# Optimization experiments

Hardware: AMD Instinct MI355X
Metric: run time of the kernel (lower is better)

The kernel has to match this reference:

```python
import jax, jax.numpy as jnp
import numpy as np

# Dimensions (match init_kwargs / input_specs)
B, S, F, H = 4, 1024, 1024, 16
D = F // H            # head_dim = 64
MAX_LEN = 1024        # synthesizer random-table length


def setup_inputs() -> dict:
    key = jax.random.key(0)
    ks = jax.random.split(key, 7)
    init = 0.02  # stand-in for lecun-style kernel init scale
    rn = lambda k, shape, sc=init: (jax.random.normal(k, shape, jnp.float32) * sc)
    return {
        "inputs_q": jax.random.normal(ks[0], (B, S, F), jnp.float32),
        "Wq": rn(ks[1], (F, H, D)), "bq": jnp.zeros((H, D), jnp.float32),
        "Wk": rn(ks[2], (F, H, D)), "bk": jnp.zeros((H, D), jnp.float32),
        "Wv": rn(ks[3], (F, H, D)), "bv": jnp.zeros((H, D), jnp.float32),
        "R":  rn(ks[4], (H, MAX_LEN, MAX_LEN)),   # 'random' synthesizer param
        "Wo": rn(ks[5], (H, D, F)), "bo": jnp.zeros((F,), jnp.float32),
    }


def reference(inputs_q, Wq, bq, Wk, bk, Wv, bv, R, Wo, bo):
    # Self-attention: inputs_kv = inputs_q. QKV projections (DenseGeneral axis=-1 -> (H, D)).
    q = jnp.einsum('bqf,fhd->bqhd', inputs_q, Wq) + bq
    k = jnp.einsum('bkf,fhd->bkhd', inputs_q, Wk) + bk
    v = jnp.einsum('bkf,fhd->bkhd', inputs_q, Wv) + bv

    qlen, kvlen = q.shape[1], k.shape[1]
    q = q / jnp.sqrt(jnp.asarray(D, q.dtype))

    # QK^T scores [b, h, q, k] + additive synthetic random weights (broadcast over batch).
    scores = jnp.einsum('bqhd,bkhd->bhqk', q, k) + R[None, :, :qlen, :kvlen]

    # softmax over the attention (kv) axis; deterministic (dropout_rate = 0.0)
    attn = jax.nn.softmax(scores, axis=-1)

    # weighted values, back to [b, q, h, d]
    y = jnp.einsum('bhqk,bkhd->bqhd', attn, v)

    # output DenseGeneral over (heads, head_dim) -> features
    return jnp.einsum('bqhd,hdf->bqf', y, Wo) + bo
```

## Files before the change

kernel.cpp:

```cpp
#include <hip/hip_runtime.h>
#include <hip/hip_bf16.h>

typedef __bf16 bf16;
typedef __bf16 bf16x8 __attribute__((ext_vector_type(8)));
typedef float f32x4 __attribute__((ext_vector_type(4)));

typedef __attribute__((address_space(1))) const void as1_const_void;
typedef __attribute__((address_space(3))) void as3_void;

#define LOG2E 1.44269504088896340736f

__device__ __forceinline__ void gload_lds16(const bf16* g, bf16* l) {
    __builtin_amdgcn_global_load_lds((as1_const_void*)g, (as3_void*)l, 16, 0, 0);
}

__device__ __forceinline__ f32x4 mfma_bf16(bf16x8 a, bf16x8 b, f32x4 c) {
    return __builtin_amdgcn_mfma_f32_16x16x32_bf16(a, b, c, 0, 0, 0);
}

__global__ __launch_bounds__(256) void cvt_f32_bf16(const float* in, bf16* out, int n) {
    int i = (blockIdx.x * 256 + threadIdx.x) * 8;
    if (i >= n) return;
    f32x4 a = *(const f32x4*)(in + i);
    f32x4 b = *(const f32x4*)(in + i + 4);
    bf16x8 o;
#pragma unroll
    for (int j = 0; j < 4; ++j) { o[j] = (bf16)a[j]; o[4 + j] = (bf16)b[j]; }
    *(bf16x8*)(out + i) = o;
}

__global__ __launch_bounds__(256) void transcvt4(const float* i0, const float* i1,
                                                 const float* i2, const float* i3,
                                                 bf16* o0, bf16* o1, bf16* o2, bf16* o3) {
    const float* in;
    bf16* out;
    switch (blockIdx.z) {
        case 0: in = i0; out = o0; break;
        case 1: in = i1; out = o1; break;
        case 2: in = i2; out = o2; break;
        default: in = i3; out = o3; break;
    }
    __shared__ bf16 tile[64][72];
    const int t = threadIdx.x;
    const int r0 = blockIdx.y * 64, c0 = blockIdx.x * 64;
#pragma unroll
    for (int i = 0; i < 4; ++i) {
        int e = t * 4 + i * 1024;
        int r = e >> 6, c = e & 63;
        f32x4 v = *(const f32x4*)(in + (size_t)(r0 + r) * 1024 + c0 + c);
#pragma unroll
        for (int jj = 0; jj < 4; ++jj) tile[c + jj][r] = (bf16)v[jj];
    }
    __syncthreads();
#pragma unroll
    for (int i = 0; i < 2; ++i) {
        int e = t * 8 + i * 2048;
        int r = e >> 6, c = e & 63;
        bf16x8 v;
#pragma unroll
        for (int jj = 0; jj < 8; ++jj) v[jj] = tile[r][c + jj];
        *(bf16x8*)(out + (size_t)(c0 + r) * 1024 + r0 + c) = v;
    }
}

struct GArg { const bf16* BT; const float* bias; void* out; float scale; int mode; };
struct GArgs { GArg g[3]; };

__global__ __launch_bounds__(256) void gemm_bt(const bf16* A, GArgs args, int M, int N, int K) {
    GArg ga = args.g[blockIdx.z];
    __shared__ bf16 As[128 * 32];
    __shared__ bf16 Bs[128 * 32];
    const int t = threadIdx.x;
    const int w = t >> 6, l = t & 63;
    const int fr = l & 15, fq = l >> 4;
    const int brow = blockIdx.y * 128, bcol = blockIdx.x * 128;
    const int wr = w >> 1, wc = w & 1;

    f32x4 acc[4][4] = {};

    const int srow = t >> 2;
    const int scol = (t & 3) * 8;
    const bf16* gA = A + (size_t)(brow + srow) * K + scol;
    const bf16* gB = ga.BT + (size_t)(bcol + srow) * K + scol;

    for (int k0 = 0; k0 < K; k0 += 32) {
        __syncthreads();
        gload_lds16(gA + k0,           As + w * 512);
        gload_lds16(gA + 64 * K + k0,  As + 2048 + w * 512);
        gload_lds16(gB + k0,           Bs + w * 512);
        gload_lds16(gB + 64 * K + k0,  Bs + 2048 + w * 512);
        __syncthreads();

        bf16x8 af[4], bfr[4];
#pragma unroll
        for (int m = 0; m < 4; ++m)
            af[m] = *(const bf16x8*)(As + (wr * 64 + m * 16 + fr) * 32 + fq * 8);
#pragma unroll
        for (int n = 0; n < 4; ++n)
            bfr[n] = *(const bf16x8*)(Bs + (wc * 64 + n * 16 + fr) * 32 + fq * 8);
#pragma unroll
        for (int m = 0; m < 4; ++m)
#pragma unroll
            for (int n = 0; n < 4; ++n)
                acc[m][n] = mfma_bf16(af[m], bfr[n], acc[m][n]);
    }

    float biasv[4];
#pragma unroll
    for (int n = 0; n < 4; ++n)
        biasv[n] = ga.bias[bcol + wc * 64 + n * 16 + fr];

#pragma unroll
    for (int m = 0; m < 4; ++m) {
#pragma unroll
        for (int n = 0; n < 4; ++n) {
            int gcol = bcol + wc * 64 + n * 16 + fr;
#pragma unroll
            for (int j = 0; j < 4; ++j) {
                int grow = brow + wr * 64 + m * 16 + fq * 4 + j;
                float v = (acc[m][n][j] + biasv[n]) * ga.scale;
                if (ga.mode == 0) {
                    ((bf16*)ga.out)[(size_t)grow * N + gcol] = (bf16)v;
                } else if (ga.mode == 1) {
                    int b = grow >> 10, s = grow & 1023;
                    int h = gcol >> 6, d = gcol & 63;
                    ((bf16*)ga.out)[(((size_t)(b * 16 + h)) * 64 + d) * 1024 + s] = (bf16)v;
                } else {
                    ((float*)ga.out)[(size_t)grow * N + gcol] = v;
                }
            }
        }
    }
}

__global__ __launch_bounds__(256) void attn_fused(const bf16* q, const bf16* k,
                                                  const bf16* vT, const float* R, bf16* y) {
    const int bx = blockIdx.x;
    const int qt = bx & 15, h = (bx >> 4) & 15, b = bx >> 8;
    const int q0 = qt * 64;
    const int t = threadIdx.x, w = t >> 6, l = t & 63;
    const int fr = l & 15, fq = l >> 4;

    __shared__ bf16 Ks[64 * 64];
    __shared__ bf16 VTs[64 * 64];
    __shared__ bf16 Ps[4 * 16 * 64];

    const bf16* qbase = q + (((size_t)(b * 1024 + q0 + w * 16 + fr)) * 16 + h) * 64;
    bf16x8 Qf[2];
    Qf[0] = *(const bf16x8*)(qbase + fq * 8);
    Qf[1] = *(const bf16x8*)(qbase + 32 + fq * 8);

    bf16x8 onesB;
#pragma unroll
    for (int i = 0; i < 8; ++i) onesB[i] = (bf16)1.0f;

    f32x4 Yacc[4] = {};
    f32x4 Lacc = {};

    const bf16*  vtb = vT + ((size_t)(b * 16 + h)) * 64 * 1024;
    const bf16*  kb  = k + ((size_t)(b * 1024)) * 1024 + h * 64;
    const float* Rb  = R + ((size_t)h) * 1024 * 1024 + (size_t)(q0 + w * 16) * 1024;

    const int srow = t >> 3;
    const int scb  = (t & 7) ^ (srow & 7);

    float rp[4][4];
#pragma unroll
    for (int n = 0; n < 4; ++n)
#pragma unroll
        for (int j = 0; j < 4; ++j)
            rp[n][j] = Rb[(size_t)(fq * 4 + j) * 1024 + n * 16 + fr];

    for (int kv0 = 0; kv0 < 1024; kv0 += 64) {
        __syncthreads();

        gload_lds16(kb + (size_t)(kv0 + srow) * 1024 + scb * 8,       Ks + w * 512);
        gload_lds16(kb + (size_t)(kv0 + srow + 32) * 1024 + scb * 8,  Ks + 2048 + w * 512);
        gload_lds16(vtb + (size_t)srow * 1024 + kv0 + scb * 8,        VTs + w * 512);
        gload_lds16(vtb + (size_t)(srow + 32) * 1024 + kv0 + scb * 8, VTs + 2048 + w * 512);

        f32x4 S[4];
#pragma unroll
        for (int n = 0; n < 4; ++n)
#pragma unroll
            for (int j = 0; j < 4; ++j)
                S[n][j] = rp[n][j];
        {
            int kvn = (kv0 + 64) & 1023;
#pragma unroll
            for (int n = 0; n < 4; ++n)
#pragma unroll
                for (int j = 0; j < 4; ++j)
                    rp[n][j] = Rb[(size_t)(fq * 4 + j) * 1024 + kvn + n * 16 + fr];
        }

        __syncthreads();

#pragma unroll
        for (int n = 0; n < 4; ++n) {
            const int row = n * 16 + fr;
            const int sw = (row & 7) << 4;
            const char* kr = (const char*)Ks + row * 128;
            bf16x8 K0 = *(const bf16x8*)(kr + ((fq * 16) ^ sw));
            bf16x8 K1 = *(const bf16x8*)(kr + ((64 + fq * 16) ^ sw));
            S[n] = mfma_bf16(Qf[0], K0, S[n]);
            S[n] = mfma_bf16(Qf[1], K1, S[n]);
        }

#pragma unroll
        for (int n = 0; n < 4; ++n)
#pragma unroll
            for (int j = 0; j < 4; ++j)
                S[n][j] = exp2f(S[n][j] * LOG2E);

        char* pwb = (char*)(Ps + w * 1024);
#pragma unroll
        for (int n = 0; n < 4; ++n)
#pragma unroll
            for (int j = 0; j < 4; ++j) {
                const int row = fq * 4 + j;
                *(bf16*)(pwb + ((row * 128 + (n * 16 + fr) * 2) ^ ((row & 7) << 4))) =
                    (bf16)S[n][j];
            }

        const int swp = (fr & 7) << 4;
        bf16x8 Pa0 = *(const bf16x8*)(pwb + (fr * 128 + ((fq * 16) ^ swp)));
        bf16x8 Pa1 = *(const bf16x8*)(pwb + (fr * 128 + ((64 + fq * 16) ^ swp)));

#pragma unroll
        for (int nd = 0; nd < 4; ++nd) {
            const int row = nd * 16 + fr;
            const int sw = (row & 7) << 4;
            const char* vr = (const char*)VTs + row * 128;
            bf16x8 V0 = *(const bf16x8*)(vr + ((fq * 16) ^ sw));
            bf16x8 V1 = *(const bf16x8*)(vr + ((64 + fq * 16) ^ sw));
            Yacc[nd] = mfma_bf16(Pa0, V0, Yacc[nd]);
            Yacc[nd] = mfma_bf16(Pa1, V1, Yacc[nd]);
        }
        Lacc = mfma_bf16(Pa0, onesB, Lacc);
        Lacc = mfma_bf16(Pa1, onesB, Lacc);
    }

    bf16* yb = y + (((size_t)(b * 1024 + q0 + w * 16)) * 16 + h) * 64;
    float inv[4];
#pragma unroll
    for (int j = 0; j < 4; ++j) inv[j] = 1.0f / Lacc[j];
#pragma unroll
    for (int nd = 0; nd < 4; ++nd)
#pragma unroll
        for (int j = 0; j < 4; ++j) {
            float ov = Yacc[nd][j] * inv[j];
            yb[(size_t)(fq * 4 + j) * 1024 + nd * 16 + fr] = (bf16)ov;
        }
}

extern "C" void kernel_launch(void* const* d_in, const int* in_sizes, int n_in,
                              void* d_out, int out_size, void* d_ws, size_t ws_size,
                              hipStream_t stream) {
    const float* Xq = (const float*)d_in[0];
    const float* Wq = (const float*)d_in[1];
    const float* bq = (const float*)d_in[2];
    const float* Wk = (const float*)d_in[3];
    const float* bk = (const float*)d_in[4];
    const float* Wv = (const float*)d_in[5];
    const float* bv = (const float*)d_in[6];
    const float* R  = (const float*)d_in[7];
    const float* Wo = (const float*)d_in[8];
    const float* bo = (const float*)d_in[9];
    float* out = (float*)d_out;

    char* ws = (char*)d_ws;
    bf16* xb  = (bf16*)(ws);
    bf16* qw  = (bf16*)(ws + (8u << 20));
    bf16* kw  = (bf16*)(ws + (16u << 20));
    bf16* vT  = (bf16*)(ws + (24u << 20));
    bf16* yw  = (bf16*)(ws + (32u << 20));
    bf16* WqT = (bf16*)(ws + (40u << 20));
    bf16* WkT = (bf16*)(ws + (42u << 20));
    bf16* WvT = (bf16*)(ws + (44u << 20));
    bf16* WoT = (bf16*)(ws + (46u << 20));

    const int NX = 4 * 1024 * 1024;
    cvt_f32_bf16<<<dim3(NX / (256 * 8)), 256, 0, stream>>>(Xq, xb, NX);
    transcvt4<<<dim3(16, 16, 4), 256, 0, stream>>>(Wq, Wk, Wv, Wo, WqT, WkT, WvT, WoT);

    GArgs g3;
    g3.g[0] = {WqT, bq, qw, 0.125f, 0};
    g3.g[1] = {WkT, bk, kw, 1.0f, 0};
    g3.g[2] = {WvT, bv, vT, 1.0f, 1};
    gemm_bt<<<dim3(8, 32, 3), 256, 0, stream>>>(xb, g3, 4096, 1024, 1024);

    attn_fused<<<dim3(1024), 256, 0, stream>>>(qw, kw, vT, R, yw);

    GArgs g1;
    g1.g[0] = {WoT, bo, out, 1.0f, 2};
    g1.g[1] = {nullptr, nullptr, nullptr, 0.0f, 0};
    g1.g[2] = {nullptr, nullptr, nullptr, 0.0f, 0};
    gemm_bt<<<dim3(8, 32, 1), 256, 0, stream>>>(yw, g1, 4096, 1024, 1024);
}
```

Baseline: 259.3 us.

## Widen GEMM K-tile with swizzled LDS and double query rows per attention block

The projection GEMM now stages 64-wide K slices instead of 32, using an XOR-swizzled LDS layout to avoid bank conflicts, so the loop runs half as many barrier-synchronised iterations. The attention kernel has each wave handle 32 query rows instead of 16. Each K/V tile loaded into LDS is therefore reused across twice as many queries, and the launch uses half as many blocks. The cost is more registers (double the S, Yacc and R-prefetch arrays), which may lower occupancy, plus fewer blocks in the attention grid.

After: 247.4 us. -4.6%, faster.

```diff
diff --git a/kernel.cpp b/kernel.cpp
--- a/kernel.cpp
+++ b/kernel.cpp
@@ -68,8 +68,8 @@
 
 __global__ __launch_bounds__(256) void gemm_bt(const bf16* A, GArgs args, int M, int N, int K) {
     GArg ga = args.g[blockIdx.z];
-    __shared__ bf16 As[128 * 32];
-    __shared__ bf16 Bs[128 * 32];
+    __shared__ bf16 As[128 * 64];
+    __shared__ bf16 Bs[128 * 64];
     const int t = threadIdx.x;
     const int w = t >> 6, l = t & 63;
     const int fr = l & 15, fq = l >> 4;
@@ -78,31 +78,44 @@
 
     f32x4 acc[4][4] = {};
 
-    const int srow = t >> 2;
-    const int scol = (t & 3) * 8;
+    const int srow = t >> 3;
+    const int scol = ((t & 7) ^ (srow & 7)) * 8;
     const bf16* gA = A + (size_t)(brow + srow) * K + scol;
     const bf16* gB = ga.BT + (size_t)(bcol + srow) * K + scol;
 
-    for (int k0 = 0; k0 < K; k0 += 32) {
+    for (int k0 = 0; k0 < K; k0 += 64) {
         __syncthreads();
-        gload_lds16(gA + k0,           As + w * 512);
-        gload_lds16(gA + 64 * K + k0,  As + 2048 + w * 512);
-        gload_lds16(gB + k0,           Bs + w * 512);
-        gload_lds16(gB + 64 * K + k0,  Bs + 2048 + w * 512);
+#pragma unroll
+        for (int i = 0; i < 4; ++i) {
+            gload_lds16(gA + (size_t)(i * 32) * K + k0, As + i * 2048 + w * 512);
+            gload_lds16(gB + (size_t)(i * 32) * K + k0, Bs + i * 2048 + w * 512);
+        }
         __syncthreads();
 
-        bf16x8 af[4], bfr[4];
-#pragma unroll
-        for (int m = 0; m < 4; ++m)
-            af[m] = *(const bf16x8*)(As + (wr * 64 + m * 16 + fr) * 32 + fq * 8);
-#pragma unroll
-        for (int n = 0; n < 4; ++n)
-            bfr[n] = *(const bf16x8*)(Bs + (wc * 64 + n * 16 + fr) * 32 + fq * 8);
-#pragma unroll
-        for (int m = 0; m < 4; ++m)
-#pragma unroll
-            for (int n = 0; n < 4; ++n)
-                acc[m][n] = mfma_bf16(af[m], bfr[n], acc[m][n]);
+        bf16x8 af[4][2], bfr[4][2];
+#pragma unroll
+        for (int m = 0; m < 4; ++m) {
+            const int row = wr * 64 + m * 16 + fr;
+            const int sw = (row & 7) << 4;
+            const char* ar = (const char*)As + row * 128;
+            af[m][0] = *(const bf16x8*)(ar + ((fq * 16) ^ sw));
+            af[m][1] = *(const bf16x8*)(ar + ((64 + fq * 16) ^ sw));
+        }
+#pragma unroll
+        for (int n = 0; n < 4; ++n) {
+            const int row = wc * 64 + n * 16 + fr;
+            const int sw = (row & 7) << 4;
+            const char* br = (const char*)Bs + row * 128;
+            bfr[n][0] = *(const bf16x8*)(br + ((fq * 16) ^ sw));
+            bfr[n][1] = *(const bf16x8*)(br + ((64 + fq * 16) ^ sw));
+        }
+#pragma unroll
+        for (int kk = 0; kk < 2; ++kk)
+#pragma unroll
+            for (int m = 0; m < 4; ++m)
+#pragma unroll
+                for (int n = 0; n < 4; ++n)
+                    acc[m][n] = mfma_bf16(af[m][kk], bfr[n][kk], acc[m][n]);
     }
 
     float biasv[4];
@@ -136,40 +149,46 @@
 __global__ __launch_bounds__(256) void attn_fused(const bf16* q, const bf16* k,
                                                   const bf16* vT, const float* R, bf16* y) {
     const int bx = blockIdx.x;
-    const int qt = bx & 15, h = (bx >> 4) & 15, b = bx >> 8;
-    const int q0 = qt * 64;
+    const int qt = bx & 7, h = (bx >> 3) & 15, b = bx >> 7;
+    const int q0 = qt * 128;
     const int t = threadIdx.x, w = t >> 6, l = t & 63;
     const int fr = l & 15, fq = l >> 4;
+    const int qr = q0 + w * 32;
 
     __shared__ bf16 Ks[64 * 64];
     __shared__ bf16 VTs[64 * 64];
-    __shared__ bf16 Ps[4 * 16 * 64];
-
-    const bf16* qbase = q + (((size_t)(b * 1024 + q0 + w * 16 + fr)) * 16 + h) * 64;
-    bf16x8 Qf[2];
-    Qf[0] = *(const bf16x8*)(qbase + fq * 8);
-    Qf[1] = *(const bf16x8*)(qbase + 32 + fq * 8);
+    __shared__ bf16 Ps[4 * 32 * 64];
+
+    bf16x8 Qf[2][2];
+#pragma unroll
+    for (int m = 0; m < 2; ++m) {
+        const bf16* qb = q + (((size_t)(b * 1024 + qr + m * 16 + fr)) * 16 + h) * 64;
+        Qf[m][0] = *(const bf16x8*)(qb + fq * 8);
+        Qf[m][1] = *(const bf16x8*)(qb + 32 + fq * 8);
+    }
 
     bf16x8 onesB;
 #pragma unroll
     for (int i = 0; i < 8; ++i) onesB[i] = (bf16)1.0f;
 
-    f32x4 Yacc[4] = {};
-    f32x4 Lacc = {};
+    f32x4 Yacc[2][4] = {};
+    f32x4 Lacc[2] = {};
 
     const bf16*  vtb = vT + ((size_t)(b * 16 + h)) * 64 * 1024;
     const bf16*  kb  = k + ((size_t)(b * 1024)) * 1024 + h * 64;
-    const float* Rb  = R + ((size_t)h) * 1024 * 1024 + (size_t)(q0 + w * 16) * 1024;
+    const float* Rb  = R + ((size_t)h) * 1024 * 1024 + (size_t)qr * 1024;
 
     const int srow = t >> 3;
     const int scb  = (t & 7) ^ (srow & 7);
 
-    float rp[4][4];
-#pragma unroll
-    for (int n = 0; n < 4; ++n)
-#pragma unroll
-        for (int j = 0; j < 4; ++j)
-            rp[n][j] = Rb[(size_t)(fq * 4 + j) * 1024 + n * 16 + fr];
+    float rp[2][4][4];
+#pragma unroll
+    for (int m = 0; m < 2; ++m)
+#pragma unroll
+        for (int n = 0; n < 4; ++n)
+#pragma unroll
+            for (int j = 0; j < 4; ++j)
+                rp[m][n][j] = Rb[(size_t)(m * 16 + fq * 4 + j) * 1024 + n * 16 + fr];
 
     for (int kv0 = 0; kv0 < 1024; kv0 += 64) {
         __syncthreads();
@@ -179,19 +198,23 @@
         gload_lds16(vtb + (size_t)srow * 1024 + kv0 + scb * 8,        VTs + w * 512);
         gload_lds16(vtb + (size_t)(srow + 32) * 1024 + kv0 + scb * 8, VTs + 2048 + w * 512);
 
-        f32x4 S[4];
-#pragma unroll
-        for (int n = 0; n < 4; ++n)
-#pragma unroll
-            for (int j = 0; j < 4; ++j)
-                S[n][j] = rp[n][j];
+        f32x4 S[2][4];
+#pragma unroll
+        for (int m = 0; m < 2; ++m)
+#pragma unroll
+            for (int n = 0; n < 4; ++n)
+#pragma unroll
+                for (int j = 0; j < 4; ++j)
+                    S[m][n][j] = rp[m][n][j];
         {
             int kvn = (kv0 + 64) & 1023;
 #pragma unroll
-            for (int n = 0; n < 4; ++n)
-#pragma unroll
-                for (int j = 0; j < 4; ++j)
-                    rp[n][j] = Rb[(size_t)(fq * 4 + j) * 1024 + kvn + n * 16 + fr];
+            for (int m = 0; m < 2; ++m)
+#pragma unroll
+                for (int n = 0; n < 4; ++n)
+#pragma unroll
+                    for (int j = 0; j < 4; ++j)
+                        rp[m][n][j] = Rb[(size_t)(m * 16 + fq * 4 + j) * 1024 + kvn + n * 16 + fr];
         }
 
         __syncthreads();
@@ -203,29 +226,34 @@
             const char* kr = (const char*)Ks + row * 128;
             bf16x8 K0 = *(const bf16x8*)(kr + ((fq * 16) ^ sw));
             bf16x8 K1 = *(const bf16x8*)(kr + ((64 + fq * 16) ^ sw));
-            S[n] = mfma_bf16(Qf[0], K0, S[n]);
-            S[n] = mfma_bf16(Qf[1], K1, S[n]);
-        }
-
-#pragma unroll
-        for (int n = 0; n < 4; ++n)
-#pragma unroll
-            for (int j = 0; j < 4; ++j)
-                S[n][j] = exp2f(S[n][j] * LOG2E);
-
-        char* pwb = (char*)(Ps + w * 1024);
-#pragma unroll
-        for (int n = 0; n < 4; ++n)
-#pragma unroll
-            for (int j = 0; j < 4; ++j) {
-                const int row = fq * 4 + j;
-                *(bf16*)(pwb + ((row * 128 + (n * 16 + fr) * 2) ^ ((row & 7) << 4))) =
-                    (bf16)S[n][j];
+#pragma unroll
+            for (int m = 0; m < 2; ++m) {
+                S[m][n] = mfma_bf16(Qf[m][0], K0, S[m][n]);
+                S[m][n] = mfma_bf16(Qf[m][1], K1, S[m][n]);
             }
-
-        const int swp = (fr & 7) << 4;
-        bf16x8 Pa0 = *(const bf16x8*)(pwb + (fr * 128 + ((fq * 16) ^ swp)));
-        bf16x8 Pa1 = *(const bf16x8*)(pwb + (fr * 128 + ((64 + fq * 16) ^ swp)));
+        }
+
+        char* pwb = (char*)(Ps + w * 2048);
+#pragma unroll
+        for (int m = 0; m < 2; ++m)
+#pragma unroll
+            for (int n = 0; n < 4; ++n)
+#pragma unroll
+                for (int j = 0; j < 4; ++j) {
+                    float pv = exp2f(S[m][n][j] * LOG2E);
+                    const int row = m * 16 + fq * 4 + j;
+                    *(bf16*)(pwb + ((row * 128 + (n * 16 + fr) * 2) ^ ((row & 7) << 4))) =
+                        (bf16)pv;
+                }
+
+        bf16x8 Pa[2][2];
+#pragma unroll
+        for (int m = 0; m < 2; ++m) {
+            const int row = m * 16 + fr;
+            const int sw = (row & 7) << 4;
+            Pa[m][0] = *(const bf16x8*)(pwb + (row * 128 + ((fq * 16) ^ sw)));
+            Pa[m][1] = *(const bf16x8*)(pwb + (row * 128 + ((64 + fq * 16) ^ sw)));
+        }
 
 #pragma unroll
         for (int nd = 0; nd < 4; ++nd) {
@@ -234,24 +262,33 @@
             const char* vr = (const char*)VTs + row * 128;
             bf16x8 V0 = *(const bf16x8*)(vr + ((fq * 16) ^ sw));
             bf16x8 V1 = *(const bf16x8*)(vr + ((64 + fq * 16) ^ sw));
-            Yacc[nd] = mfma_bf16(Pa0, V0, Yacc[nd]);
-            Yacc[nd] = mfma_bf16(Pa1, V1, Yacc[nd]);
-        }
-        Lacc = mfma_bf16(Pa0, onesB, Lacc);
-        Lacc = mfma_bf16(Pa1, onesB, Lacc);
-    }
-
-    bf16* yb = y + (((size_t)(b * 1024 + q0 + w * 16)) * 16 + h) * 64;
-    float inv[4];
-#pragma unroll
-    for (int j = 0; j < 4; ++j) inv[j] = 1.0f / Lacc[j];
-#pragma unroll
-    for (int nd = 0; nd < 4; ++nd)
-#pragma unroll
-        for (int j = 0; j < 4; ++j) {
-            float ov = Yacc[nd][j] * inv[j];
-            yb[(size_t)(fq * 4 + j) * 1024 + nd * 16 + fr] = (bf16)ov;
-        }
+#pragma unroll
+            for (int m = 0; m < 2; ++m) {
+                Yacc[m][nd] = mfma_bf16(Pa[m][0], V0, Yacc[m][nd]);
+                Yacc[m][nd] = mfma_bf16(Pa[m][1], V1, Yacc[m][nd]);
+            }
+        }
+#pragma unroll
+        for (int m = 0; m < 2; ++m) {
+            Lacc[m] = mfma_bf16(Pa[m][0], onesB, Lacc[m]);
+            Lacc[m] = mfma_bf16(Pa[m][1], onesB, Lacc[m]);
+        }
+    }
+
+#pragma unroll
+    for (int m = 0; m < 2; ++m) {
+        bf16* yb = y + (((size_t)(b * 1024 + qr + m * 16)) * 16 + h) * 64;
+        float inv[4];
+#pragma unroll
+        for (int j = 0; j < 4; ++j) inv[j] = 1.0f / Lacc[m][j];
+#pragma unroll
+        for (int nd = 0; nd < 4; ++nd)
+#pragma unroll
+            for (int j = 0; j < 4; ++j) {
+                float ov = Yacc[m][nd][j] * inv[j];
+                yb[(size_t)(fq * 4 + j) * 1024 + nd * 16 + fr] = (bf16)ov;
+            }
+    }
 }
 
 extern "C" void kernel_launch(void* const* d_in, const int* in_sizes, int n_in,
@@ -290,7 +327,7 @@
     g3.g[2] = {WvT, bv, vT, 1.0f, 1};
     gemm_bt<<<dim3(8, 32, 3), 256, 0, stream>>>(xb, g3, 4096, 1024, 1024);
 
-    attn_fused<<<dim3(1024), 256, 0, stream>>>(qw, kw, vT, R, yw);
+    attn_fused<<<dim3(512), 256, 0, stream>>>(qw, kw, vT, R, yw);
 
     GArgs g1;
     g1.g[0] = {WoT, bo, out, 1.0f, 2};
```
